# Optimization experiments

Hardware: AMD Instinct MI355X
Metric: run time of the kernel (lower is better)

Reference implementation:

```python
import jax, jax.numpy as jnp
import numpy as np

DIM = 1      # homological dimension
CARD = 50    # number of diagram points
H, W = 28, 28
D = 2        # len(Ip.shape)


def _cubical(X, dim=DIM, card=CARD):
    """Pure-numpy cubical persistence (gudhi semantics: lower-dim cells get the
    min of incident top-dimensional cells; finite pairs of dimension `dim`,
    positive persistence, sorted by persistence descending; returns flat
    (i,j) pixel indices of birth/death critical top cells, zero-padded to
    2*D*card int32 values). Mirrors the Cubical numpy_function in the repo."""
    X = np.asarray(X, dtype=np.float64)
    Hh, Ww = X.shape
    A, Bc = 2 * Hh - 1, 2 * Ww - 1
    n = A * Bc
    F = np.empty(n)                 # filtration value per cell
    P = np.empty(n, np.int64)       # flat pixel index of the top cell realizing F
    dms = np.empty(n, np.int64)     # cell dimension

    def cands(a, lim):
        if a % 2 == 1:
            return [(a - 1) // 2]
        return [r for r in (a // 2 - 1, a // 2) if 0 <= r < lim]

    for a in range(A):
        ris = cands(a, Hh)
        for b in range(Bc):
            cjs = cands(b, Ww)
            best = None
            bp = 0
            for r in ris:
                for c in cjs:
                    v = X[r, c]
                    if best is None or v < best:
                        best = v
                        bp = r * Ww + c
            idx = a * Bc + b
            F[idx] = best
            P[idx] = bp
            dms[idx] = (a & 1) + (b & 1)

    order = np.lexsort((np.arange(n), dms, F))   # sort by (F, dim, index)
    pos = np.empty(n, np.int64)
    pos[order] = np.arange(n)

    def faces(cell):
        a, b = divmod(cell, Bc)
        fs = []
        if a & 1:
            fs += [(a - 1) * Bc + b, (a + 1) * Bc + b]
        if b & 1:
            fs += [a * Bc + b - 1, a * Bc + b + 1]
        return fs

    # standard Z/2 boundary-matrix reduction
    Rcols = {}
    low_to_col = {}
    pairs = []
    for j in range(n):
        cell = order[j]
        col = set(int(pos[f]) for f in faces(cell))
        while col:
            l = max(col)
            k = low_to_col.get(l)
            if k is None:
                break
            col ^= Rcols[k]
        if col:
            l = max(col)
            low_to_col[l] = j
            Rcols[j] = col
            pairs.append((l, j))

    rows, pers = [], []
    for (i, j) in pairs:
        bc, dc = order[i], order[j]
        if dms[bc] != dim:
            continue
        pr = F[dc] - F[bc]
        if pr <= 0:
            continue
        rows.append((int(P[bc]), int(P[dc])))
        pers.append(pr)
    if rows:
        srt = np.argsort(np.asarray(pers))[::-1]   # persistence descending
        rows = [rows[k] for k in srt]

    inds = []
    for k in range(min(card, len(rows))):
        bi, di = rows[k]
        inds += [bi // Ww, bi % Ww, di // Ww, di % Ww]
    inds += [0] * (2 * D * card - len(inds))
    return np.asarray(inds, dtype=np.int32)


def setup_inputs() -> dict:
    key = jax.random.key(0)
    k1, k2 = jax.random.split(key)
    I = jax.random.normal(k1, (H, W, 2), dtype=jnp.float32)
    p = jax.random.normal(k2, (2, 1), dtype=jnp.float32)
    return {"I": I, "p": p}


def reference(I, p):
    # Ip = reshape(tensordot(I, p, 1), [28, 28])
    Ip = jnp.reshape(jnp.tensordot(I, p, 1), (H, W))
    inds = jax.pure_callback(
        lambda x: _cubical(np.asarray(x)),
        jax.ShapeDtypeStruct((2 * D * CARD,), jnp.int32),
        Ip,
    )
    inds = jax.lax.stop_gradient(inds).reshape(-1, D)   # [2*card, 2]
    # gather_nd(Ip, inds) then reshape to [card, 2]
    dgm = Ip[inds[:, 0], inds[:, 1]].reshape(-1, 2)
    return dgm
```

## Files before the change

kernel.cpp:

```cpp
#include <hip/hip_runtime.h>

#define IMG_H 28
#define IMG_W 28
#define AA 55
#define NCELL 3025
#define NEDGE 1512
#define NSQ 729
#define CARD 50
#define NW 24
#define CAP 160
#define BS 1024

typedef unsigned long long u64;
typedef unsigned int u32;
typedef unsigned short u16;

#define OFF_KEYSE   0
#define OFF_KEYSS   16384
#define OFF_IP      24576
#define OFF_RANKE   27712
#define OFF_RANKSQ  30736
#define OFF_COL     0
#define OFF_OWNB    30720
#define OFF_CANDA   0
#define OFF_CANDB   8192
#define OFF_BND     43008
#define OFF_EDGEF   48840
#define OFF_SQF     54888
#define OFF_LLIST2  57808
#define OFF_CURLOW  58448
#define OFF_LCNT    58768
#define OFF_PAIRLOW 60832
#define OFF_NONAPP  62296
#define OFF_SCAL    63768
#define SMEM_TOTAL  63776

__device__ __forceinline__ int edgeCid(int a, int b) {
    return (a & 1) ? (((a - 1) >> 1) * 28 + (b >> 1))
                   : (756 + (a >> 1) * 27 + ((b - 1) >> 1));
}

__device__ __forceinline__ u32 sortable(float f) {
    u32 fb = __float_as_uint(f);
    return (fb & 0x80000000u) ? ~fb : (fb | 0x80000000u);
}
__device__ __forceinline__ float unsortable(u32 v) {
    return __uint_as_float((v & 0x80000000u) ? (v & 0x7FFFFFFFu) : ~v);
}

__device__ __forceinline__ u64 shflx64(u64 v, int s) {
    u32 lo = __shfl_xor((u32)v, s, 64);
    u32 hi = __shfl_xor((u32)(v >> 32), s, 64);
    return ((u64)hi << 32) | lo;
}

__device__ __forceinline__ void cswapDir(u64& a, u64& b, bool up) {
    u64 mn = a < b ? a : b, mx = a < b ? b : a;
    a = up ? mn : mx; b = up ? mx : mn;
}

__device__ __forceinline__ u64 bstage(u64 v, int i, int s, int size) {
    u64 p = shflx64(v, s);
    bool keepmin = (((i & size) == 0) == ((i & s) == 0));
    return keepmin ? (v < p ? v : p) : (v > p ? v : p);
}

__device__ __forceinline__ void sessA(u64& r0, u64& r1, int i0) {
    for (int size = 2; size <= 64; size <<= 1)
        for (int s = size >> 1; s; s >>= 1) {
            r0 = bstage(r0, i0, s, size);
            r1 = bstage(r1, i0 + 64, s, size);
        }
}
__device__ __forceinline__ void sessB(u64& r0, u64& r1, int i0, int size) {
    bool asc = ((i0 & size) == 0);
    { u64 mn = r0 < r1 ? r0 : r1, mx = r0 < r1 ? r1 : r0;
      r0 = asc ? mn : mx; r1 = asc ? mx : mn; }
    for (int s = 32; s; s >>= 1) {
        bool keep = (asc == ((i0 & s) == 0));
        u64 p0 = shflx64(r0, s);
        r0 = keep ? (r0 < p0 ? r0 : p0) : (r0 > p0 ? r0 : p0);
        u64 p1 = shflx64(r1, s);
        r1 = keep ? (r1 < p1 ? r1 : p1) : (r1 > p1 ? r1 : p1);
    }
}

template<int G>
__device__ __forceinline__ void fusedClassicArr(u64* arr, int nElem) {
    const int nG = nElem / G;
    for (int gid = (int)threadIdx.x; gid < nG; gid += BS) {
        int high = gid >> 7, low = gid & 127;
        bool up = ((high & 1) == 0);
        int base = high * G * 128 + low;
        u64 k[G];
        #pragma unroll
        for (int g = 0; g < G; ++g) k[g] = arr[base + g * 128];
        #pragma unroll
        for (int d = G / 2; d >= 1; d >>= 1)
            #pragma unroll
            for (int g = 0; g < G; ++g)
                if (!(g & d)) cswapDir(k[g], k[g | d], up);
        #pragma unroll
        for (int g = 0; g < G; ++g) arr[base + g * 128] = k[g];
    }
}

__device__ __forceinline__ void sessWin(u64* kE, u64* kS, int i0, int size, bool hasS) {
    u64 a = kE[i0], b = kE[i0 + 64];
    sessB(a, b, i0, size);
    kE[i0] = a; kE[i0 + 64] = b;
    if (hasS) {
        u64 c = kS[i0], d = kS[i0 + 64];
        sessB(c, d, i0, size);
        kS[i0] = c; kS[i0 + 64] = d;
    }
}

__device__ __forceinline__ u64 lstage(u64 v, int lane, int s, bool up) {
    u64 p = shflx64(v, s);
    bool keepmin = (up == ((lane & s) == 0));
    return keepmin ? (v < p ? v : p) : (v > p ? v : p);
}

__device__ __forceinline__ u64 sort64(u64 v, int lane) {
    for (int size = 2; size <= 32; size <<= 1)
        for (int s = size >> 1; s; s >>= 1)
            v = lstage(v, lane, s, (lane & size) == 0);
    for (int s = 32; s; s >>= 1)
        v = lstage(v, lane, s, true);
    return v;
}
__device__ __forceinline__ u64 merge64(u64 a, u64 b, int lane) {
    u64 br = shflx64(b, 63);
    u64 m = a < br ? a : br;
    for (int s = 32; s; s >>= 1)
        m = lstage(m, lane, s, true);
    return m;
}

__device__ __forceinline__ void xorOwner(u64 o, u64& w, int lane, const u64* col) {
    if (!(o >> 63)) {
        #pragma unroll
        for (int q = 0; q < 4; ++q) {
            int rr = (int)((o >> (12 * q)) & 0xFFFull);
            if ((rr >> 6) == lane) w ^= 1ull << (rr & 63);
        }
    } else {
        int s = (int)(o & 0xFFFFull);
        if (lane < NW) w ^= col[s * NW + lane];
    }
}

__device__ __forceinline__ int findLow(u64 w, int lane) {
    u64 mask = __ballot(w != 0ull);
    if (mask == 0ull) return 0xFFFE;
    int L = 63 - __builtin_clzll(mask);
    int cand = (lane << 6) + 63 - __builtin_clzll(w | 1ull);
    return __builtin_amdgcn_readlane(cand, L);
}

__global__ __launch_bounds__(BS) void cubical_kernel(const float* __restrict__ I,
                                                     const float* __restrict__ p,
                                                     float* __restrict__ out) {
    __shared__ __align__(16) char smem[SMEM_TOTAL];
    u64*    keysE   = (u64*)(smem + OFF_KEYSE);
    u64*    keysS   = (u64*)(smem + OFF_KEYSS);
    float*  Ip      = (float*)(smem + OFF_IP);
    u16*    rankE   = (u16*)(smem + OFF_RANKE);
    u16*    rankSq  = (u16*)(smem + OFF_RANKSQ);
    u64*    col     = (u64*)(smem + OFF_COL);
    u64*    ownerBnd= (u64*)(smem + OFF_OWNB);
    u64*    candA   = (u64*)(smem + OFF_CANDA);
    u64*    candB   = (u64*)(smem + OFF_CANDB);
    u64*    bnd     = (u64*)(smem + OFF_BND);
    float*  edgeFr  = (float*)(smem + OFF_EDGEF);
    float*  sqF     = (float*)(smem + OFF_SQF);
    u16*    lList2  = (u16*)(smem + OFF_LLIST2);
    u16*    curLow  = (u16*)(smem + OFF_CURLOW);
    int*    lCntArr = (int*)(smem + OFF_LCNT);
    u16*    pairLow = (u16*)(smem + OFF_PAIRLOW);
    u16*    nonapp  = (u16*)(smem + OFF_NONAPP);
    float*  padvP   = (float*)(smem + OFF_SCAL);
    int*    Mp      = (int*)(smem + OFF_SCAL + 4);

    const int tid = threadIdx.x;
    const int wave = tid >> 6, lane = tid & 63;

    const float p0 = p[0], p1 = p[1];
    for (int i = tid; i < IMG_H * IMG_W; i += BS) {
        float v = I[2 * i] * p0 + I[2 * i + 1] * p1;
        Ip[i] = v;
        if (i == 0) *padvP = v;
    }
    for (int i = 1512 + tid; i < 2048; i += BS) keysE[i] = ~0ull;
    for (int i = 729 + tid; i < 1024; i += BS) keysS[i] = ~0ull;
    __syncthreads();

    for (int idx = tid; idx < NCELL; idx += BS) {
        int a = idx / AA, b = idx % AA;
        int da = a & 1, db = b & 1;
        int dim = da + db;
        if (dim == 0) continue;
        int r0, r1, c0, c1;
        if (da) { r0 = r1 = (a - 1) >> 1; }
        else    { r1 = a >> 1; r0 = (a == 0) ? r1 : r1 - 1; }
        if (db) { c0 = c1 = (b - 1) >> 1; }
        else    { c1 = b >> 1; c0 = (b == 0) ? c1 : c1 - 1; }
        float best = Ip[r0 * IMG_W + c0];
        best = fminf(best, Ip[r0 * IMG_W + c1]);
        best = fminf(best, Ip[r1 * IMG_W + c0]);
        best = fminf(best, Ip[r1 * IMG_W + c1]);
        u64 key = ((u64)sortable(best) << 12) | (u32)idx;
        if (dim == 1) keysE[edgeCid(a, b)] = key;
        else          keysS[((a - 1) >> 1) * 27 + ((b - 1) >> 1)] = key;
    }
    __syncthreads();

    {
        const int eB = wave * 128 + lane;
        const bool hasS = (wave < 8);
        {
            u64 a = keysE[eB], b = keysE[eB + 64];
            sessA(a, b, eB);
            sessB(a, b, eB, 128);
            keysE[eB] = a; keysE[eB + 64] = b;
            if (hasS) {
                u64 c = keysS[eB], d = keysS[eB + 64];
                sessA(c, d, eB);
                sessB(c, d, eB, 128);
                keysS[eB] = c; keysS[eB + 64] = d;
            }
        }
        __syncthreads();
        fusedClassicArr<2>(keysE, 2048);
        fusedClassicArr<2>(keysS, 1024);
        __syncthreads();
        sessWin(keysE, keysS, eB, 256, hasS);
        __syncthreads();
        fusedClassicArr<4>(keysE, 2048);
        fusedClassicArr<4>(keysS, 1024);
        __syncthreads();
        sessWin(keysE, keysS, eB, 512, hasS);
        __syncthreads();
        fusedClassicArr<8>(keysE, 2048);
        fusedClassicArr<8>(keysS, 1024);
        __syncthreads();
        sessWin(keysE, keysS, eB, 1024, hasS);
        __syncthreads();
        fusedClassicArr<16>(keysE, 2048);
        __syncthreads();
        sessWin(keysE, keysS, eB, 2048, false);
        __syncthreads();
    }

    for (int r = tid; r < NEDGE; r += BS) {
        u64 k = keysE[r];
        int idx = (int)(k & 0xFFFull);
        int a = idx / AA, b = idx % AA;
        rankE[edgeCid(a, b)] = (u16)r;
        edgeFr[r] = unsortable((u32)(k >> 12));
    }
    for (int r = tid; r < NSQ; r += BS) {
        u64 k = keysS[r];
        int idx = (int)(k & 0xFFFull);
        int a = idx / AA, b = idx % AA;
        rankSq[((a - 1) >> 1) * 27 + ((b - 1) >> 1)] = (u16)r;
        sqF[r] = unsortable((u32)(k >> 12));
    }
    __syncthreads();

    for (int j = tid; j < NSQ; j += BS) {
        int sidx = (int)(keysS[j] & 0xFFFull);
        int a = sidx / AA, b = sidx % AA;
        int ec[4] = { sidx - AA, sidx + AA, sidx - 1, sidx + 1 };
        int er[4];
        er[0] = rankE[edgeCid(a - 1, b)];
        er[1] = rankE[edgeCid(a + 1, b)];
        er[2] = rankE[edgeCid(a, b - 1)];
        er[3] = rankE[edgeCid(a, b + 1)];
        bnd[j] = (u64)er[0] | ((u64)er[1] << 16) | ((u64)er[2] << 32) | ((u64)er[3] << 48);
        int bq = 0;
        if (er[1] > er[bq]) bq = 1;
        if (er[2] > er[bq]) bq = 2;
        if (er[3] > er[bq]) bq = 3;
        int ecell = ec[bq];
        int x = ecell / AA, y = ecell % AA;
        u32 rmin = 0xFFFFFFFFu;
        if (x & 1) {
            if (y >= 2)  rmin = rankSq[((x - 1) >> 1) * 27 + ((y - 2) >> 1)];
            if (y <= 52) { u32 r2 = rankSq[((x - 1) >> 1) * 27 + (y >> 1)]; rmin = min(rmin, r2); }
        } else {
            if (x >= 2)  rmin = rankSq[((x - 2) >> 1) * 27 + ((y - 1) >> 1)];
            if (x <= 52) { u32 r2 = rankSq[(x >> 1) * 27 + ((y - 1) >> 1)]; rmin = min(rmin, r2); }
        }
        pairLow[j] = (rmin == (u32)j) ? (u16)(0x8000u | er[bq]) : (u16)0xFFFFu;
    }
    __syncthreads();

    for (int i = tid; i < 1536; i += BS) ownerBnd[i] = ~0ull;
    __syncthreads();
    for (int j = tid; j < NSQ; j += BS) {
        u16 pl = pairLow[j];
        if (pl != 0xFFFFu) {
            u64 bd = bnd[j];
            u64 e = (bd & 0xFFFull) | (((bd >> 16) & 0xFFFull) << 12)
                  | (((bd >> 32) & 0xFFFull) << 24) | (((bd >> 48) & 0xFFFull) << 36);
            ownerBnd[pl & 0x7FFF] = e;
        }
    }
    if (tid < 64) {
        int cnt = 0;
        for (int base = 0; base < NSQ; base += 64) {
            int j = base + lane;
            bool f = (j < NSQ) && (pairLow[j] == 0xFFFFu);
            u64 m = __ballot(f);
            int pfx = __popcll(m & ((1ull << lane) - 1ull));
            if (f) nonapp[cnt + pfx] = (u16)j;
            cnt += __popcll(m);
        }
        if (lane == 0) *Mp = (cnt > CAP) ? CAP : cnt;
    }
    __syncthreads();
    const int M = *Mp;

    for (int idx = tid; idx < M * NW; idx += BS) {
        int slot = idx / NW, w = idx - slot * NW;
        u64 bd = bnd[nonapp[slot]];
        u64 x = 0ull;
        #pragma unroll
        for (int q = 0; q < 4; ++q) {
            int rr = (int)((bd >> (16 * q)) & 0xFFFFull);
            if ((rr >> 6) == w) x ^= 1ull << (rr & 63);
        }
        col[idx] = x;
    }
    if (tid < 256) lCntArr[tid] = 0;
    if (tid < M) {
        u64 bd = bnd[nonapp[tid]];
        int mx = 0;
        #pragma unroll
        for (int q = 0; q < 4; ++q) {
            int rr = (int)((bd >> (16 * q)) & 0xFFFFull);
            if (rr > mx) mx = rr;
        }
        curLow[tid] = (u16)mx;
        lList2[tid] = (u16)tid;
    }
    if (tid == 0) lCntArr[0] = M;
    __syncthreads();

    {
        const int nWaves = BS / 64;
        for (int round = 0; round < 255; ++round) {
            const int nL = lCntArr[round];
            if (nL == 0) break;
            const u16* inL = lList2 + (round & 1) * CAP;
            u16* outL = lList2 + ((round + 1) & 1) * CAP;
            int* outC = lCntArr + (round + 1);
            for (int li = wave; li < nL; li += nWaves) {
                int slot = (int)inL[li];
                const u64 myEnc = (1ull << 63) | (u64)slot;
                u64 w = (lane < NW) ? col[slot * NW + lane] : 0ull;
                int low = (int)curLow[slot];
                while (low != 0xFFFE) {
                    u64 o = *(volatile u64*)&ownerBnd[low];
                    if (o < myEnc) {
                        xorOwner(o, w, lane, col);
                        low = findLow(w, lane);
                    } else {
                        if (lane < NW) col[slot * NW + lane] = w;
                        __threadfence_block();
                        u64 got = 0;
                        if (lane == 0) {
                            u64 cur = *(volatile u64*)&ownerBnd[low];
                            while (myEnc < cur) {
                                u64 prev = atomicCAS(&ownerBnd[low], cur, myEnc);
                                if (prev == cur) {
                                    if (cur != ~0ull) {
                                        int ix = atomicAdd(outC, 1);
                                        outL[ix] = (u16)(cur & 0xFFFFull);
                                    }
                                    break;
                                }
                                cur = prev;
                            }
                            got = cur;
                        }
                        u32 glo = __builtin_amdgcn_readlane((u32)got, 0);
                        u32 ghi = __builtin_amdgcn_readlane((u32)(got >> 32), 0);
                        got = ((u64)ghi << 32) | glo;
                        if (got < myEnc) {
                            xorOwner(got, w, lane, col);
                            low = findLow(w, lane);
                        } else break;
                    }
                }
                if (lane == 0) curLow[slot] = (u16)low;
                if (lane < NW) col[slot * NW + lane] = w;
            }
            __syncthreads();
        }
    }
    if (tid < M) {
        u16 cl = curLow[tid];
        pairLow[nonapp[tid]] = (cl == 0xFFFEu) ? (u16)0xFFFDu : cl;
    }
    __syncthreads();

    {
        if (wave < 12) {
            int i = wave * 64 + lane;
            u64 key = ~0ull;
            if (i < NSQ) {
                int pl = (int)pairLow[i];
                if (pl != 0xFFFD && pl != 0xFFFF) {
                    int low = pl & 0x7FFF;
                    double pr = (double)sqF[i] - (double)edgeFr[low];
                    if (pr > 0.0) {
                        u64 bits = (u64)__double_as_longlong(pr);
                        key = ~((bits & ~0xFFFull) | (u64)(u32)i);
                    }
                }
            }
            candA[wave * 64 + lane] = sort64(key, lane);
        }
        __syncthreads();
        if (wave < 6) {
            u64 a = candA[(2 * wave) * 64 + lane];
            u64 b = candA[(2 * wave + 1) * 64 + lane];
            candB[wave * 64 + lane] = merge64(a, b, lane);
        }
        __syncthreads();
        if (wave < 3) {
            u64 a = candB[(2 * wave) * 64 + lane];
            u64 b = candB[(2 * wave + 1) * 64 + lane];
            candA[wave * 64 + lane] = merge64(a, b, lane);
        }
        __syncthreads();
        if (wave == 0) {
            u64 a = candA[lane], b = candA[64 + lane], c = candA[128 + lane];
            u64 f = merge64(merge64(a, b, lane), c, lane);
            if (lane < CARD) {
                float bv, dv;
                if (f != ~0ull) {
                    u64 kb = ~f;
                    int j = (int)(kb & 0xFFFull);
                    int low = (int)pairLow[j] & 0x7FFF;
                    bv = edgeFr[low];
                    dv = sqF[j];
                } else {
                    bv = *padvP; dv = *padvP;
                }
                out[2 * lane]     = bv;
                out[2 * lane + 1] = dv;
            }
        }
    }
}

extern "C" void kernel_launch(void* const* d_in, const int* in_sizes, int n_in,
                              void* d_out, int out_size, void* d_ws, size_t ws_size,
                              hipStream_t stream) {
    const float* I = (const float*)d_in[0];
    const float* p = (const float*)d_in[1];
    float* out = (float*)d_out;
    hipLaunchKernelGGL(cubical_kernel, dim3(1), dim3(BS), 0, stream, I, p, out);
}
```

Before: 99.71 us.

## Replace round-based reduction with per-wave evicted-column chaining, dropping block barriers

```diff
diff --git a/kernel.cpp b/kernel.cpp
--- a/kernel.cpp
+++ b/kernel.cpp
@@ -27,9 +27,7 @@
 #define OFF_BND     43008
 #define OFF_EDGEF   48840
 #define OFF_SQF     54888
-#define OFF_LLIST2  57808
 #define OFF_CURLOW  58448
-#define OFF_LCNT    58768
 #define OFF_PAIRLOW 60832
 #define OFF_NONAPP  62296
 #define OFF_SCAL    63768
@@ -175,9 +173,7 @@
     u64*    bnd     = (u64*)(smem + OFF_BND);
     float*  edgeFr  = (float*)(smem + OFF_EDGEF);
     float*  sqF     = (float*)(smem + OFF_SQF);
-    u16*    lList2  = (u16*)(smem + OFF_LLIST2);
     u16*    curLow  = (u16*)(smem + OFF_CURLOW);
-    int*    lCntArr = (int*)(smem + OFF_LCNT);
     u16*    pairLow = (u16*)(smem + OFF_PAIRLOW);
     u16*    nonapp  = (u16*)(smem + OFF_NONAPP);
     float*  padvP   = (float*)(smem + OFF_SCAL);
@@ -334,7 +330,6 @@
         }
         col[idx] = x;
     }
-    if (tid < 256) lCntArr[tid] = 0;
     if (tid < M) {
         u64 bd = bnd[nonapp[tid]];
         int mx = 0;
@@ -344,62 +339,56 @@
             if (rr > mx) mx = rr;
         }
         curLow[tid] = (u16)mx;
-        lList2[tid] = (u16)tid;
-    }
-    if (tid == 0) lCntArr[0] = M;
+    }
     __syncthreads();
 
     {
         const int nWaves = BS / 64;
-        for (int round = 0; round < 255; ++round) {
-            const int nL = lCntArr[round];
-            if (nL == 0) break;
-            const u16* inL = lList2 + (round & 1) * CAP;
-            u16* outL = lList2 + ((round + 1) & 1) * CAP;
-            int* outC = lCntArr + (round + 1);
-            for (int li = wave; li < nL; li += nWaves) {
-                int slot = (int)inL[li];
-                const u64 myEnc = (1ull << 63) | (u64)slot;
-                u64 w = (lane < NW) ? col[slot * NW + lane] : 0ull;
-                int low = (int)curLow[slot];
-                while (low != 0xFFFE) {
-                    u64 o = *(volatile u64*)&ownerBnd[low];
-                    if (o < myEnc) {
-                        xorOwner(o, w, lane, col);
-                        low = findLow(w, lane);
-                    } else {
-                        if (lane < NW) col[slot * NW + lane] = w;
-                        __threadfence_block();
-                        u64 got = 0;
-                        if (lane == 0) {
-                            u64 cur = *(volatile u64*)&ownerBnd[low];
-                            while (myEnc < cur) {
-                                u64 prev = atomicCAS(&ownerBnd[low], cur, myEnc);
-                                if (prev == cur) {
-                                    if (cur != ~0ull) {
-                                        int ix = atomicAdd(outC, 1);
-                                        outL[ix] = (u16)(cur & 0xFFFFull);
-                                    }
-                                    break;
-                                }
-                                cur = prev;
-                            }
-                            got = cur;
-                        }
-                        u32 glo = __builtin_amdgcn_readlane((u32)got, 0);
-                        u32 ghi = __builtin_amdgcn_readlane((u32)(got >> 32), 0);
-                        got = ((u64)ghi << 32) | glo;
-                        if (got < myEnc) {
-                            xorOwner(got, w, lane, col);
-                            low = findLow(w, lane);
-                        } else break;
+        for (int li = wave; li < M; li += nWaves) {
+            int slot = li;
+            u64 myEnc = (1ull << 63) | (u64)slot;
+            u64 w = (lane < NW) ? col[slot * NW + lane] : 0ull;
+            int low = (int)curLow[slot];
+            for (;;) {
+                if (low == 0xFFFE) {
+                    if (lane == 0) curLow[slot] = (u16)0xFFFE;
+                    break;
+                }
+                u64 o = *(volatile u64*)&ownerBnd[low];
+                if (o < myEnc) {
+                    xorOwner(o, w, lane, col);
+                    low = findLow(w, lane);
+                    continue;
+                }
+                if (lane < NW) col[slot * NW + lane] = w;
+                __threadfence_block();
+                u64 got = 0;
+                if (lane == 0) {
+                    u64 cur = *(volatile u64*)&ownerBnd[low];
+                    while (myEnc < cur) {
+                        u64 prev = atomicCAS(&ownerBnd[low], cur, myEnc);
+                        if (prev == cur) break;
+                        cur = prev;
                     }
+                    got = cur;
+                }
+                u32 glo = __builtin_amdgcn_readlane((u32)got, 0);
+                u32 ghi = __builtin_amdgcn_readlane((u32)(got >> 32), 0);
+                got = ((u64)ghi << 32) | glo;
+                if (got < myEnc) {
+                    xorOwner(got, w, lane, col);
+                    low = findLow(w, lane);
+                    continue;
                 }
                 if (lane == 0) curLow[slot] = (u16)low;
-                if (lane < NW) col[slot * NW + lane] = w;
+                if (got == ~0ull) break;
+                __threadfence_block();
+                slot = (int)(got & 0xFFFFull);
+                myEnc = got;
+                w = (lane < NW) ? col[slot * NW + lane] : 0ull;
             }
-            __syncthreads();
-        }
+        }
+        __syncthreads();
     }
     if (tid < M) {
         u16 cl = curLow[tid];
```

New measurement: 95.16 us. 4.6% less time.
